# Performance work log

Hardware: AMD Instinct MI355X
Metric: run time of the kernel (lower is better)

The kernel has to match this reference:

```python
import jax, jax.numpy as jnp
import numpy as np

B, S, D, H = 4, 2048, 1024, 16
Dh = D // H
MAX_WAVELENGTH = 10000.0


def apply_rope(x, positions, head_dim):
    # x: [B, S, H, Dh], positions: [B, S]
    fraction = 2.0 * jnp.arange(head_dim // 2, dtype=jnp.float32) / head_dim
    timescale = MAX_WAVELENGTH ** fraction                     # [Dh/2]
    sinusoid = positions[..., None].astype(jnp.float32) / timescale  # [B, S, Dh/2]
    sinusoid = sinusoid[..., None, :]                          # [B, S, 1, Dh/2]
    sin, cos = jnp.sin(sinusoid), jnp.cos(sinusoid)
    first, second = jnp.split(x, 2, axis=-1)
    out = jnp.concatenate([first * cos - second * sin,
                           second * cos + first * sin], axis=-1)
    return out.astype(x.dtype)


def setup_inputs() -> dict:
    key = jax.random.key(0)
    k0, k1, k2, k3, k4 = jax.random.split(key, 5)
    inputs = jax.random.normal(k0, (B, S, D), dtype=jnp.float32)
    segment_positions = jnp.broadcast_to(jnp.arange(S, dtype=jnp.int32), (B, S))
    # causal mask, broadcastable over heads: [B, 1, S, S]
    mask = jnp.broadcast_to(jnp.tril(jnp.ones((S, S), dtype=bool))[None, None], (B, 1, S, S))
    std = 0.02
    w_q = jax.random.normal(k1, (D, H, Dh), dtype=jnp.float32) * std
    w_k = jax.random.normal(k2, (D, H, Dh), dtype=jnp.float32) * std
    w_v = jax.random.normal(k3, (D, H, Dh), dtype=jnp.float32) * std
    w_out = jax.random.normal(k4, (H, Dh, D), dtype=jnp.float32) * std
    return {"inputs": inputs, "w_q": w_q, "w_k": w_k, "w_v": w_v,
            "w_out": w_out, "segment_positions": segment_positions, "mask": mask}


def reference(inputs, w_q, w_k, w_v, w_out, segment_positions, mask):
    # QKV projections: [B, S, D] x [D, H, Dh] -> [B, S, H, Dh]
    q = jnp.einsum('bsd,dhk->bshk', inputs, w_q)
    k = jnp.einsum('bsd,dhk->bshk', inputs, w_k)
    v = jnp.einsum('bsd,dhk->bshk', inputs, w_v)
    q = apply_rope(q, segment_positions, Dh)
    k = apply_rope(k, segment_positions, Dh)
    q = q / jnp.sqrt(jnp.asarray(Dh, dtype=q.dtype))
    attn = jnp.einsum('bqhd,bkhd->bhqk', q, k)                 # [B, H, S, S]
    big_neg = jnp.finfo(attn.dtype).min
    attn = jnp.where(mask, attn, big_neg)
    attn = jax.nn.softmax(attn, axis=-1)
    x = jnp.einsum('bhqk,bkhd->bqhd', attn, v)                 # [B, S, H, Dh]
    return jnp.einsum('bqhd,hdm->bqm', x, w_out)               # [B, S, D]
```

## Files before the change

### kernel.cpp

```cpp
#include <hip/hip_runtime.h>
#include <stdint.h>
#include <math.h>

#define S_LEN 2048
#define DMODEL 1024
#define NHEAD 16
#define DHEAD 64
#define BATCH 4
#define MROWS (BATCH * S_LEN)

typedef __attribute__((ext_vector_type(8))) short bf16x8;
typedef __attribute__((ext_vector_type(4))) float f32x4;

#define MFMA16(a, b, c) __builtin_amdgcn_mfma_f32_16x16x32_bf16(a, b, c, 0, 0, 0)

__device__ __forceinline__ unsigned short f2b(float f) {
  union { float f; unsigned u; } v; v.f = f;
  unsigned u = v.u;
  return (unsigned short)((u + 0x7FFFu + ((u >> 16) & 1u)) >> 16);
}
__device__ __forceinline__ unsigned pkrn(float a, float b) {
  unsigned ua = __float_as_uint(a) + 0x8000u;
  unsigned ub = __float_as_uint(b) + 0x8000u;
  return __builtin_amdgcn_perm(ub, ua, 0x07060302);
}

__device__ __forceinline__ void async16(const void* g, void* l) {
  __builtin_amdgcn_global_load_lds((const __attribute__((address_space(1))) void*)g,
                                   (__attribute__((address_space(3))) void*)l,
                                   16, 0, 0);
}

__global__ __launch_bounds__(256) void cvt_kernel(const float4* __restrict__ in,
                                                  unsigned short* __restrict__ out,
                                                  int n4) {
  int i = blockIdx.x * 256 + threadIdx.x;
  if (i < n4) {
    float4 v = in[i];
    ushort4 o;
    o.x = f2b(v.x); o.y = f2b(v.y); o.z = f2b(v.z); o.w = f2b(v.w);
    *(ushort4*)(out + 4 * (size_t)i) = o;
  }
}

struct TP4 { const float* s[4]; unsigned short* d[4]; };
__global__ __launch_bounds__(256) void transpose_cvt4(TP4 p) {
  const float* in = p.s[blockIdx.z];
  unsigned short* out = p.d[blockIdx.z];
  __shared__ float T[64][65];
  int r0 = blockIdx.y * 64, c0 = blockIdx.x * 64;
  int t = threadIdx.x;
  int c = t & 63, rr = t >> 6;
#pragma unroll
  for (int i = 0; i < 16; i++) {
    int r = i * 4 + rr;
    T[r][c] = in[(size_t)(r0 + r) * 1024 + c0 + c];
  }
  __syncthreads();
  int r2 = t & 63, cc = t >> 6;
#pragma unroll
  for (int i = 0; i < 16; i++) {
    int c2 = i * 4 + cc;
    out[(size_t)(c0 + c2) * 1024 + r0 + r2] = f2b(T[r2][c2]);
  }
}

__global__ __launch_bounds__(256) void gemm_qkv(const unsigned short* __restrict__ A,
                                                const unsigned short* __restrict__ Bt,
                                                unsigned short* __restrict__ Qr,
                                                unsigned short* __restrict__ Kr,
                                                unsigned short* __restrict__ Vt,
                                                const int* __restrict__ pos) {
  constexpr int K = 1024;
  __shared__ unsigned short As[128 * 64];
  __shared__ unsigned short Bs[128 * 64];
  const int bm = blockIdx.y * 128, bn = blockIdx.x * 128;
  const int t = threadIdx.x;
  const int wave = t >> 6, lane = t & 63, quad = lane >> 4, l16 = lane & 15;
  const int wm = (wave >> 1) * 64, wn = (wave & 1) * 64;
  f32x4 acc[4][4] = {};
  const int srow = lane >> 3;
  const int gcol = (((lane & 7) ^ srow)) * 8;
  const unsigned short* Ag = A + (size_t)(bm + wave * 32 + srow) * K + gcol;
  const unsigned short* Bg = Bt + (size_t)(bn + wave * 32 + srow) * K + gcol;
  unsigned short* AsW = &As[(wave * 32) * 64];
  unsigned short* BsW = &Bs[(wave * 32) * 64];
  const int rsw = l16 & 7;

  for (int k0 = 0; k0 < K; k0 += 64) {
    __syncthreads();
#pragma unroll
    for (int i = 0; i < 4; i++) {
      async16(Ag + (size_t)(i * 8) * K + k0, AsW + i * 8 * 64);
      async16(Bg + (size_t)(i * 8) * K + k0, BsW + i * 8 * 64);
    }
    __syncthreads();
#pragma unroll
    for (int kk = 0; kk < 2; kk++) {
      const int sl = ((kk * 4 + quad) ^ rsw) << 3;
      bf16x8 af[4], bfr[4];
#pragma unroll
      for (int mt = 0; mt < 4; mt++)
        af[mt] = *(const bf16x8*)&As[(wm + mt * 16 + l16) * 64 + sl];
#pragma unroll
      for (int nt = 0; nt < 4; nt++)
        bfr[nt] = *(const bf16x8*)&Bs[(wn + nt * 16 + l16) * 64 + sl];
#pragma unroll
      for (int mt = 0; mt < 4; mt++)
#pragma unroll
        for (int nt = 0; nt < 4; nt++)
          acc[mt][nt] = MFMA16(af[mt], bfr[nt], acc[mt][nt]);
    }
  }

  const int cb = bn + wn;
  if (cb >= 2048) {
    const int h = (cb - 2048) >> 6;
#pragma unroll
    for (int mt = 0; mt < 4; mt++)
#pragma unroll
      for (int nt = 0; nt < 4; nt++) {
        int row = bm + wm + mt * 16 + quad * 4;
        int b = row >> 11, s = row & (S_LEN - 1);
        int dh = nt * 16 + l16;
        ushort4 w4;
        w4.x = f2b(acc[mt][nt][0]); w4.y = f2b(acc[mt][nt][1]);
        w4.z = f2b(acc[mt][nt][2]); w4.w = f2b(acc[mt][nt][3]);
        *(ushort4*)&Vt[((size_t)(b * NHEAD + h) * DHEAD + dh) * S_LEN + s] = w4;
      }
  } else {
    const bool isQ = cb < 1024;
    unsigned short* dst0 = isQ ? Qr : Kr;
    const float scl = isQ ? 0.18033688011112042f : 1.0f;
    const int h = (cb >> 6) & 15;
    const float LT = 0.28782313662425572f;
    float it0 = __expf(-(float)l16 * LT);
    float it1 = __expf(-(float)(16 + l16) * LT);
#pragma unroll
    for (int mt = 0; mt < 4; mt++) {
#pragma unroll
      for (int r = 0; r < 4; r++) {
        int row = bm + wm + mt * 16 + quad * 4 + r;
        int b = row >> 11, s = row & (S_LEN - 1);
        float p = (float)pos[row];
        float a0 = p * it0, a1 = p * it1;
        float sn0 = __sinf(a0), cs0 = __cosf(a0);
        float sn1 = __sinf(a1), cs1 = __cosf(a1);
        float x0 = acc[mt][0][r], x1 = acc[mt][1][r];
        float x2 = acc[mt][2][r], x3 = acc[mt][3][r];
        float o0 = (x0 * cs0 - x2 * sn0) * scl;
        float o2 = (x2 * cs0 + x0 * sn0) * scl;
        float o1 = (x1 * cs1 - x3 * sn1) * scl;
        float o3 = (x3 * cs1 + x1 * sn1) * scl;
        unsigned short* dst =
            dst0 + ((size_t)(b * NHEAD + h) * S_LEN + s) * DHEAD;
        dst[0 * 16 + l16] = f2b(o0);
        dst[1 * 16 + l16] = f2b(o1);
        dst[2 * 16 + l16] = f2b(o2);
        dst[3 * 16 + l16] = f2b(o3);
      }
    }
  }
}

__global__ __launch_bounds__(256) void gemm_out(const unsigned short* __restrict__ A,
                                                const unsigned short* __restrict__ Bt,
                                                float* __restrict__ C) {
  constexpr int K = 1024, N = 1024;
  __shared__ unsigned short As[128 * 64];
  __shared__ unsigned short Bs[128 * 64];
  const int bm = blockIdx.y * 128, bn = blockIdx.x * 128;
  const int t = threadIdx.x;
  const int wave = t >> 6, lane = t & 63, quad = lane >> 4, l16 = lane & 15;
  const int wm = (wave >> 1) * 64, wn = (wave & 1) * 64;
  f32x4 acc[4][4] = {};
  const int srow = lane >> 3;
  const int gcol = (((lane & 7) ^ srow)) * 8;
  const unsigned short* Ag = A + (size_t)(bm + wave * 32 + srow) * K + gcol;
  const unsigned short* Bg = Bt + (size_t)(bn + wave * 32 + srow) * K + gcol;
  unsigned short* AsW = &As[(wave * 32) * 64];
  unsigned short* BsW = &Bs[(wave * 32) * 64];
  const int rsw = l16 & 7;

  for (int k0 = 0; k0 < K; k0 += 64) {
    __syncthreads();
#pragma unroll
    for (int i = 0; i < 4; i++) {
      async16(Ag + (size_t)(i * 8) * K + k0, AsW + i * 8 * 64);
      async16(Bg + (size_t)(i * 8) * K + k0, BsW + i * 8 * 64);
    }
    __syncthreads();
#pragma unroll
    for (int kk = 0; kk < 2; kk++) {
      const int sl = ((kk * 4 + quad) ^ rsw) << 3;
      bf16x8 af[4], bfr[4];
#pragma unroll
      for (int mt = 0; mt < 4; mt++)
        af[mt] = *(const bf16x8*)&As[(wm + mt * 16 + l16) * 64 + sl];
#pragma unroll
      for (int nt = 0; nt < 4; nt++)
        bfr[nt] = *(const bf16x8*)&Bs[(wn + nt * 16 + l16) * 64 + sl];
#pragma unroll
      for (int mt = 0; mt < 4; mt++)
#pragma unroll
        for (int nt = 0; nt < 4; nt++)
          acc[mt][nt] = MFMA16(af[mt], bfr[nt], acc[mt][nt]);
    }
  }
#pragma unroll
  for (int mt = 0; mt < 4; mt++)
#pragma unroll
    for (int nt = 0; nt < 4; nt++)
#pragma unroll
      for (int r = 0; r < 4; r++) {
        int row = bm + wm + mt * 16 + quad * 4 + r;
        int col = bn + wn + nt * 16 + l16;
        C[(size_t)row * N + col] = acc[mt][nt][r];
      }
}

__global__ __launch_bounds__(256) void flash_kernel(const unsigned short* __restrict__ Qr,
                                                    const unsigned short* __restrict__ Kr,
                                                    const unsigned short* __restrict__ Vt,
                                                    unsigned short* __restrict__ Xat) {
  const int idx = blockIdx.x;
  const int qt = 31 - (idx >> 6);
  const int bh = idx & 63;
  const unsigned short* Qh = Qr + (size_t)bh * S_LEN * DHEAD;
  const unsigned short* Kh = Kr + (size_t)bh * S_LEN * DHEAD;
  const unsigned short* Vh = Vt + (size_t)bh * DHEAD * S_LEN;
  __shared__ unsigned short Ks[2][64 * 64];
  __shared__ unsigned short Vs[2][64 * 64];
  __shared__ unsigned short Pt[4][16 * 64];
  const int t = threadIdx.x, wave = t >> 6, lane = t & 63;
  const int quad = lane >> 4, l16 = lane & 15;
  const int srow = lane >> 3;
  const int gcol = (((lane & 7) ^ srow)) * 8;
  const int rsw = l16 & 7;
  const int q0 = qt * 64;
  const int qr = q0 + wave * 16 + l16;

  bf16x8 qf0 = *(const bf16x8*)(Qh + (size_t)qr * DHEAD + quad * 8);
  bf16x8 qf1 = *(const bf16x8*)(Qh + (size_t)qr * DHEAD + 32 + quad * 8);

  f32x4 o[4] = {};
  float l = 0.f;
  unsigned short* PtW = &Pt[wave][0];
  const int c0 = (quad ^ rsw) << 3;
  const int c1 = ((4 + quad) ^ rsw) << 3;
  const int q1b = quad >> 1, qlo4 = (quad & 1) * 4;
  const int pr = l16 * 64;

  auto stage = [&](int kt, int buf) {
    const int k0 = kt * 64;
#pragma unroll
    for (int i = 0; i < 2; i++) {
      async16(Kh + (size_t)(k0 + wave * 16 + i * 8 + srow) * DHEAD + gcol,
              &Ks[buf][(wave * 16 + i * 8) * 64]);
      async16(Vh + (size_t)(wave * 16 + i * 8 + srow) * S_LEN + k0 + gcol,
              &Vs[buf][(wave * 16 + i * 8) * 64]);
    }
  };

  auto compute = [&](int cur, bool diag, int k0) {
    const unsigned short* K_ = Ks[cur];
    const unsigned short* V_ = Vs[cur];
    f32x4 sc[4] = {};
#pragma unroll
    for (int nt = 0; nt < 4; nt++) {
      bf16x8 kb0 = *(const bf16x8*)&K_[(nt * 16 + l16) * 64 + c0];
      bf16x8 kb1 = *(const bf16x8*)&K_[(nt * 16 + l16) * 64 + c1];
      sc[nt] = MFMA16(kb0, qf0, sc[nt]);
      sc[nt] = MFMA16(kb1, qf1, sc[nt]);
    }
#pragma unroll
    for (int nt = 0; nt < 4; nt++) {
      float p0, p1, p2, p3;
      if (diag) {
        int kg = k0 + nt * 16 + quad * 4;
        p0 = (kg + 0 > qr) ? 0.f : exp2f(sc[nt][0]);
        p1 = (kg + 1 > qr) ? 0.f : exp2f(sc[nt][1]);
        p2 = (kg + 2 > qr) ? 0.f : exp2f(sc[nt][2]);
        p3 = (kg + 3 > qr) ? 0.f : exp2f(sc[nt][3]);
      } else {
        p0 = exp2f(sc[nt][0]);
        p1 = exp2f(sc[nt][1]);
        p2 = exp2f(sc[nt][2]);
        p3 = exp2f(sc[nt][3]);
      }
      l += (p0 + p1) + (p2 + p3);
      uint2 w; w.x = pkrn(p0, p1); w.y = pkrn(p2, p3);
      const int slot = ((nt * 2 + q1b) ^ rsw) << 3;
      *(uint2*)&PtW[pr + slot + qlo4] = w;
    }
#pragma unroll
    for (int kk = 0; kk < 2; kk++) {
      bf16x8 pb = *(const bf16x8*)&PtW[pr + (((kk * 4 + quad) ^ rsw) << 3)];
#pragma unroll
      for (int nt = 0; nt < 4; nt++) {
        bf16x8 vb = *(const bf16x8*)&V_[(nt * 16 + l16) * 64 + (kk == 0 ? c0 : c1)];
        o[nt] = MFMA16(vb, pb, o[nt]);
      }
    }
  };

  stage(0, 0);
  int kt = 0;
  for (; kt + 2 <= qt; kt += 2) {
    __syncthreads();
    stage(kt + 1, 1);
    compute(0, false, kt * 64);
    __syncthreads();
    stage(kt + 2, 0);
    compute(1, false, (kt + 1) * 64);
  }
  if (kt < qt) {
    __syncthreads();
    stage(qt, 1);
    compute(0, false, kt * 64);
    __syncthreads();
    compute(1, true, qt * 64);
  } else {
    __syncthreads();
    compute(0, true, qt * 64);
  }

  l += __shfl_xor(l, 16);
  l += __shfl_xor(l, 32);
  const float iv = 1.0f / l;
  const int b = bh >> 4, h = bh & 15;
  unsigned short* d = Xat + (size_t)(b * S_LEN + qr) * DMODEL + h * DHEAD;
#pragma unroll
  for (int nt = 0; nt < 4; nt++) {
    ushort4 w4;
    w4.x = f2b(o[nt][0] * iv); w4.y = f2b(o[nt][1] * iv);
    w4.z = f2b(o[nt][2] * iv); w4.w = f2b(o[nt][3] * iv);
    *(ushort4*)(d + nt * 16 + quad * 4) = w4;
  }
}

extern "C" void kernel_launch(void* const* d_in, const int* in_sizes, int n_in,
                              void* d_out, int out_size, void* d_ws, size_t ws_size,
                              hipStream_t stream) {
  const float* x = (const float*)d_in[0];
  const float* wq = (const float*)d_in[1];
  const float* wk = (const float*)d_in[2];
  const float* wv = (const float*)d_in[3];
  const float* wo = (const float*)d_in[4];
  const int* pos = (const int*)d_in[5];
  float* out = (float*)d_out;
  char* ws = (char*)d_ws;

  const size_t EL_X = (size_t)MROWS * DMODEL;
  const size_t EL_W = (size_t)DMODEL * DMODEL;
  unsigned short* Xb = (unsigned short*)ws;
  unsigned short* Wqkv = Xb + EL_X;
  unsigned short* WoT = Wqkv + 3 * EL_W;
  unsigned short* Qr = WoT + EL_W;
  unsigned short* Kr = Qr + EL_X;
  unsigned short* Vt = Kr + EL_X;
  unsigned short* Xat = Vt + EL_X;

  cvt_kernel<<<(int)(EL_X / 4 / 256), 256, 0, stream>>>((const float4*)x, Xb,
                                                        (int)(EL_X / 4));
  TP4 tp;
  tp.s[0] = wq; tp.d[0] = Wqkv;
  tp.s[1] = wk; tp.d[1] = Wqkv + EL_W;
  tp.s[2] = wv; tp.d[2] = Wqkv + 2 * EL_W;
  tp.s[3] = wo; tp.d[3] = WoT;
  dim3 tg(16, 16, 4);
  transpose_cvt4<<<tg, 256, 0, stream>>>(tp);
  dim3 gq(24, 64);
  gemm_qkv<<<gq, 256, 0, stream>>>(Xb, Wqkv, Qr, Kr, Vt, pos);
  flash_kernel<<<2048, 256, 0, stream>>>(Qr, Kr, Vt, Xat);
  dim3 gg(8, 64);
  gemm_out<<<gg, 256, 0, stream>>>(Xat, WoT, out);
}
```

Baseline: 293.2 us.

## Process two 64-row query tiles per flash block to reuse K/V tiles

Each flash attention block now handles 128 query rows split into two 64-row groups that share every staged K/V tile, halving the grid to 1024 blocks. Score MFMAs for both groups reuse the same K fragments, and the diagonal handling is split so group A masks at tile 2qt and group B at tile 2qt+1. This aims to reduce LDS loads, global K/V traffic and barrier overhead per query row. In exchange it doubles accumulator registers (launch bound set to 3 blocks/SM) and has fewer, longer blocks, which may worsen tail balance.

Result: faster. 285.3 us (-2.7%).

```diff
diff --git a/kernel.cpp b/kernel.cpp
--- a/kernel.cpp
+++ b/kernel.cpp
@@ -219,12 +219,12 @@
       }
 }
 
-__global__ __launch_bounds__(256) void flash_kernel(const unsigned short* __restrict__ Qr,
-                                                    const unsigned short* __restrict__ Kr,
-                                                    const unsigned short* __restrict__ Vt,
-                                                    unsigned short* __restrict__ Xat) {
+__global__ __launch_bounds__(256, 3) void flash_kernel(const unsigned short* __restrict__ Qr,
+                                                       const unsigned short* __restrict__ Kr,
+                                                       const unsigned short* __restrict__ Vt,
+                                                       unsigned short* __restrict__ Xat) {
   const int idx = blockIdx.x;
-  const int qt = 31 - (idx >> 6);
+  const int qt = 15 - (idx >> 6);
   const int bh = idx & 63;
   const unsigned short* Qh = Qr + (size_t)bh * S_LEN * DHEAD;
   const unsigned short* Kh = Kr + (size_t)bh * S_LEN * DHEAD;
@@ -237,14 +237,17 @@
   const int srow = lane >> 3;
   const int gcol = (((lane & 7) ^ srow)) * 8;
   const int rsw = l16 & 7;
-  const int q0 = qt * 64;
-  const int qr = q0 + wave * 16 + l16;
-
-  bf16x8 qf0 = *(const bf16x8*)(Qh + (size_t)qr * DHEAD + quad * 8);
-  bf16x8 qf1 = *(const bf16x8*)(Qh + (size_t)qr * DHEAD + 32 + quad * 8);
-
-  f32x4 o[4] = {};
-  float l = 0.f;
+  const int q0 = qt * 128;
+  const int qrA = q0 + wave * 16 + l16;
+  const int qrB = qrA + 64;
+
+  bf16x8 qfA0 = *(const bf16x8*)(Qh + (size_t)qrA * DHEAD + quad * 8);
+  bf16x8 qfA1 = *(const bf16x8*)(Qh + (size_t)qrA * DHEAD + 32 + quad * 8);
+  bf16x8 qfB0 = *(const bf16x8*)(Qh + (size_t)qrB * DHEAD + quad * 8);
+  bf16x8 qfB1 = *(const bf16x8*)(Qh + (size_t)qrB * DHEAD + 32 + quad * 8);
+
+  f32x4 oA[4] = {}, oB[4] = {};
+  float lA = 0.f, lB = 0.f;
   unsigned short* PtW = &Pt[wave][0];
   const int c0 = (quad ^ rsw) << 3;
   const int c1 = ((4 + quad) ^ rsw) << 3;
@@ -262,26 +265,17 @@
     }
   };
 
-  auto compute = [&](int cur, bool diag, int k0) {
-    const unsigned short* K_ = Ks[cur];
-    const unsigned short* V_ = Vs[cur];
-    f32x4 sc[4] = {};
-#pragma unroll
-    for (int nt = 0; nt < 4; nt++) {
-      bf16x8 kb0 = *(const bf16x8*)&K_[(nt * 16 + l16) * 64 + c0];
-      bf16x8 kb1 = *(const bf16x8*)&K_[(nt * 16 + l16) * 64 + c1];
-      sc[nt] = MFMA16(kb0, qf0, sc[nt]);
-      sc[nt] = MFMA16(kb1, qf1, sc[nt]);
-    }
+  auto softpv = [&](const unsigned short* V_, f32x4* sc, f32x4* o, float& l,
+                    int qr_, bool diag, int k0) {
 #pragma unroll
     for (int nt = 0; nt < 4; nt++) {
       float p0, p1, p2, p3;
       if (diag) {
         int kg = k0 + nt * 16 + quad * 4;
-        p0 = (kg + 0 > qr) ? 0.f : exp2f(sc[nt][0]);
-        p1 = (kg + 1 > qr) ? 0.f : exp2f(sc[nt][1]);
-        p2 = (kg + 2 > qr) ? 0.f : exp2f(sc[nt][2]);
-        p3 = (kg + 3 > qr) ? 0.f : exp2f(sc[nt][3]);
+        p0 = (kg + 0 > qr_) ? 0.f : exp2f(sc[nt][0]);
+        p1 = (kg + 1 > qr_) ? 0.f : exp2f(sc[nt][1]);
+        p2 = (kg + 2 > qr_) ? 0.f : exp2f(sc[nt][2]);
+        p3 = (kg + 3 > qr_) ? 0.f : exp2f(sc[nt][3]);
       } else {
         p0 = exp2f(sc[nt][0]);
         p1 = exp2f(sc[nt][1]);
@@ -304,38 +298,67 @@
     }
   };
 
+  auto computeAB = [&](int cur, int k0, bool adiag) {
+    const unsigned short* K_ = Ks[cur];
+    const unsigned short* V_ = Vs[cur];
+    f32x4 scA[4] = {}, scB[4] = {};
+#pragma unroll
+    for (int nt = 0; nt < 4; nt++) {
+      bf16x8 kb0 = *(const bf16x8*)&K_[(nt * 16 + l16) * 64 + c0];
+      bf16x8 kb1 = *(const bf16x8*)&K_[(nt * 16 + l16) * 64 + c1];
+      scA[nt] = MFMA16(kb0, qfA0, scA[nt]);
+      scA[nt] = MFMA16(kb1, qfA1, scA[nt]);
+      scB[nt] = MFMA16(kb0, qfB0, scB[nt]);
+      scB[nt] = MFMA16(kb1, qfB1, scB[nt]);
+    }
+    softpv(V_, scA, oA, lA, qrA, adiag, k0);
+    softpv(V_, scB, oB, lB, qrB, false, k0);
+  };
+
   stage(0, 0);
+  const int kmax = 2 * qt;
   int kt = 0;
-  for (; kt + 2 <= qt; kt += 2) {
+  for (; kt < kmax; kt += 2) {
     __syncthreads();
     stage(kt + 1, 1);
-    compute(0, false, kt * 64);
+    computeAB(0, kt * 64, false);
     __syncthreads();
     stage(kt + 2, 0);
-    compute(1, false, (kt + 1) * 64);
-  }
-  if (kt < qt) {
-    __syncthreads();
-    stage(qt, 1);
-    compute(0, false, kt * 64);
-    __syncthreads();
-    compute(1, true, qt * 64);
-  } else {
-    __syncthreads();
-    compute(0, true, qt * 64);
-  }
-
-  l += __shfl_xor(l, 16);
-  l += __shfl_xor(l, 32);
-  const float iv = 1.0f / l;
+    computeAB(1, (kt + 1) * 64, false);
+  }
+  __syncthreads();
+  stage(kmax + 1, 1);
+  computeAB(0, kmax * 64, true);
+  __syncthreads();
+  {
+    const unsigned short* K_ = Ks[1];
+    const unsigned short* V_ = Vs[1];
+    f32x4 scB[4] = {};
+#pragma unroll
+    for (int nt = 0; nt < 4; nt++) {
+      bf16x8 kb0 = *(const bf16x8*)&K_[(nt * 16 + l16) * 64 + c0];
+      bf16x8 kb1 = *(const bf16x8*)&K_[(nt * 16 + l16) * 64 + c1];
+      scB[nt] = MFMA16(kb0, qfB0, scB[nt]);
+      scB[nt] = MFMA16(kb1, qfB1, scB[nt]);
+    }
+    softpv(V_, scB, oB, lB, qrB, true, (kmax + 1) * 64);
+  }
+
+  lA += __shfl_xor(lA, 16); lA += __shfl_xor(lA, 32);
+  lB += __shfl_xor(lB, 16); lB += __shfl_xor(lB, 32);
+  const float ivA = 1.0f / lA, ivB = 1.0f / lB;
   const int b = bh >> 4, h = bh & 15;
-  unsigned short* d = Xat + (size_t)(b * S_LEN + qr) * DMODEL + h * DHEAD;
+  unsigned short* dA = Xat + (size_t)(b * S_LEN + qrA) * DMODEL + h * DHEAD;
+  unsigned short* dB = Xat + (size_t)(b * S_LEN + qrB) * DMODEL + h * DHEAD;
 #pragma unroll
   for (int nt = 0; nt < 4; nt++) {
-    ushort4 w4;
-    w4.x = f2b(o[nt][0] * iv); w4.y = f2b(o[nt][1] * iv);
-    w4.z = f2b(o[nt][2] * iv); w4.w = f2b(o[nt][3] * iv);
-    *(ushort4*)(d + nt * 16 + quad * 4) = w4;
+    ushort4 wa, wb;
+    wa.x = f2b(oA[nt][0] * ivA); wa.y = f2b(oA[nt][1] * ivA);
+    wa.z = f2b(oA[nt][2] * ivA); wa.w = f2b(oA[nt][3] * ivA);
+    wb.x = f2b(oB[nt][0] * ivB); wb.y = f2b(oB[nt][1] * ivB);
+    wb.z = f2b(oB[nt][2] * ivB); wb.w = f2b(oB[nt][3] * ivB);
+    *(ushort4*)(dA + nt * 16 + quad * 4) = wa;
+    *(ushort4*)(dB + nt * 16 + quad * 4) = wb;
   }
 }
 
@@ -372,7 +395,7 @@
   transpose_cvt4<<<tg, 256, 0, stream>>>(tp);
   dim3 gq(24, 64);
   gemm_qkv<<<gq, 256, 0, stream>>>(Xb, Wqkv, Qr, Kr, Vt, pos);
-  flash_kernel<<<2048, 256, 0, stream>>>(Qr, Kr, Vt, Xat);
+  flash_kernel<<<1024, 256, 0, stream>>>(Qr, Kr, Vt, Xat);
   dim3 gg(8, 64);
   gemm_out<<<gg, 256, 0, stream>>>(Xat, WoT, out);
 }
```
